# Kernel optimization log

Hardware: AMD Instinct MI355X
Metric: run time of the kernel (lower is better)

## Reference

```python
import jax, jax.numpy as jnp
import numpy as np

B, N, IN_F = 16, 1024, 256
HEADS, OUT_F = 4, 64
NEG_SLOPE = 0.2
CLAMP_MIN = -1e9
MASK_VAL = -9e15


def setup_inputs() -> dict:
    key = jax.random.key(0)
    k1, k2, k3, k4 = jax.random.split(key, 4)
    x = jax.random.normal(k1, (B, N, IN_F), dtype=jnp.float32)
    adj = jax.random.randint(k2, (B, N, N), 0, 2, dtype=jnp.int32)
    # Linear weight, stored as (in, heads*out) so y = x @ W (xavier-uniform scale)
    lim_w = float(np.sqrt(6.0 / (IN_F + HEADS * OUT_F)))
    W = jax.random.uniform(k3, (IN_F, HEADS * OUT_F), dtype=jnp.float32,
                           minval=-lim_w, maxval=lim_w)
    lim_a = float(np.sqrt(6.0 / (2 * OUT_F + HEADS)))
    a = jax.random.uniform(k4, (2 * OUT_F, HEADS), dtype=jnp.float32,
                           minval=-lim_a, maxval=lim_a)
    return {"x": x, "adj": adj, "W": W, "a": a}


def reference(x, adj, W, a):
    Bs, Ns, _ = x.shape
    # Projection: (B,N,H,D)
    h = (x @ W).reshape(Bs, Ns, HEADS, OUT_F)
    # cat([h_i, h_j]) . a == h_i . a_src + h_j . a_dst  (exact same math, no O(N^2*2D) tensor)
    a_src, a_dst = a[:OUT_F], a[OUT_F:]          # each (D, H)
    s_src = jnp.einsum('bnhd,dh->bnh', h, a_src)  # score contribution of node i
    s_dst = jnp.einsum('bnhd,dh->bnh', h, a_dst)  # score contribution of node j
    e = jax.nn.leaky_relu(s_src[:, :, None, :] + s_dst[:, None, :, :],
                          negative_slope=NEG_SLOPE)  # (B,N,N,H)
    # match original: subtract unmasked row max, clamp, then mask, then softmax over j
    e = e - jnp.max(e, axis=2, keepdims=True)
    e = jnp.maximum(e, CLAMP_MIN)
    att = jnp.where(adj[..., None] > 0, e, MASK_VAL)
    att = jax.nn.softmax(att, axis=2)
    h_prime = jnp.einsum('bijh,bjhd->bihd', att, h)  # (B,N,H,D)
    return h_prime.reshape(Bs, Ns, HEADS * OUT_F)
```

## Files before the change

### kernel.cpp

```cpp
#include <hip/hip_runtime.h>
#include <hip/hip_bf16.h>

#define B_   16
#define N_   1024
#define INF_ 256
#define NH_  4
#define HD_  256
#define L2E  1.4426950408889634f

typedef __attribute__((ext_vector_type(8))) short short8;
typedef __attribute__((ext_vector_type(4))) float f32x4;

__device__ __forceinline__ float bf2f(unsigned short u) {
    union { unsigned int i; float f; } v; v.i = ((unsigned int)u) << 16; return v.f;
}
__device__ __forceinline__ unsigned short f2bf(float f) {
    union { float f; unsigned int i; } v; v.f = f;
    unsigned int x = v.i;
    return (unsigned short)((x + 0x7fffu + ((x >> 16) & 1u)) >> 16);
}

__global__ __launch_bounds__(256) void k_prep(const int* __restrict__ adj,
                                              const float* __restrict__ W,
                                              unsigned int* __restrict__ pb,
                                              unsigned short* __restrict__ wswz)
{
    int bx = blockIdx.x, t = threadIdx.x;
    if (bx < 2048) {
        int wave = t >> 6, lane = t & 63;
        int row = bx * 8 + wave * 2 + (lane >> 5);
        int w   = lane & 31;
        const int4* ar = (const int4*)(adj + ((long)row << 10) + w * 32);
        unsigned int u = 0;
        #pragma unroll
        for (int k = 0; k < 8; k++) {
            int4 a = ar[k];
            u |= ((unsigned)a.x) << (4 * k);
            u |= ((unsigned)a.y) << (4 * k + 1);
            u |= ((unsigned)a.z) << (4 * k + 2);
            u |= ((unsigned)a.w) << (4 * k + 3);
        }
        pb[((long)row << 5) + w] = u;
    } else {
        int slot = (bx - 2048) * 256 + t;
        int kstep = slot >> 10;
        int nt    = (slot >> 6) & 15;
        int lane  = slot & 63;
        int k0 = kstep * 32 + (lane >> 4) * 8;
        int n  = nt * 16 + (lane & 15);
        ushort4 o0, o1;
        o0.x = f2bf(W[(k0 + 0) * HD_ + n]);
        o0.y = f2bf(W[(k0 + 1) * HD_ + n]);
        o0.z = f2bf(W[(k0 + 2) * HD_ + n]);
        o0.w = f2bf(W[(k0 + 3) * HD_ + n]);
        o1.x = f2bf(W[(k0 + 4) * HD_ + n]);
        o1.y = f2bf(W[(k0 + 5) * HD_ + n]);
        o1.z = f2bf(W[(k0 + 6) * HD_ + n]);
        o1.w = f2bf(W[(k0 + 7) * HD_ + n]);
        *(ushort4*)&wswz[(long)slot * 8]     = o0;
        *(ushort4*)&wswz[(long)slot * 8 + 4] = o1;
    }
}

__global__ __launch_bounds__(256) void k_gemm_h(
    const float* __restrict__ x, const float* __restrict__ a,
    const unsigned short* __restrict__ wswz,
    unsigned short* __restrict__ hswz,
    float* __restrict__ ssrc, float* __restrict__ sdst)
{
    __shared__ unsigned short xls[16][264];
    int t = threadIdx.x;
    int blk = blockIdx.x;
    int row0 = blk * 16;
    int b  = blk >> 6;
    int n0 = row0 & 1023;

    {
        int sr = t >> 4, sc = (t & 15) * 16;
        const float* xp = x + (long)(row0 + sr) * INF_ + sc;
        float4 v0 = ((const float4*)xp)[0];
        float4 v1 = ((const float4*)xp)[1];
        float4 v2 = ((const float4*)xp)[2];
        float4 v3 = ((const float4*)xp)[3];
        ushort4 u0 = {f2bf(v0.x), f2bf(v0.y), f2bf(v0.z), f2bf(v0.w)};
        ushort4 u1 = {f2bf(v1.x), f2bf(v1.y), f2bf(v1.z), f2bf(v1.w)};
        ushort4 u2 = {f2bf(v2.x), f2bf(v2.y), f2bf(v2.z), f2bf(v2.w)};
        ushort4 u3 = {f2bf(v3.x), f2bf(v3.y), f2bf(v3.z), f2bf(v3.w)};
        *(ushort4*)&xls[sr][sc]      = u0;
        *(ushort4*)&xls[sr][sc + 4]  = u1;
        *(ushort4*)&xls[sr][sc + 8]  = u2;
        *(ushort4*)&xls[sr][sc + 12] = u3;
    }
    __syncthreads();

    int wave = t >> 6, lane = t & 63, quad = lane >> 4, l15 = lane & 15;
    f32x4 acc[4];
    #pragma unroll
    for (int i = 0; i < 4; i++) acc[i] = (f32x4){0.f, 0.f, 0.f, 0.f};

    #pragma unroll
    for (int ks = 0; ks < 8; ks++) {
        short8 af = *(const short8*)&xls[l15][ks * 32 + quad * 8];
        #pragma unroll
        for (int nt = 0; nt < 4; nt++) {
            short8 bf = *(const short8*)(wswz +
                ((long)((ks * 16 + wave * 4 + nt) * 64 + lane)) * 8);
            acc[nt] = __builtin_amdgcn_mfma_f32_16x16x32_bf16(af, bf, acc[nt], 0, 0, 0);
        }
    }

    int q0 = (quad & 1) * 4;
    int qd = ((row0 & 31) + quad * 4) >> 3;
    long bj32 = row0 >> 5;
    #pragma unroll
    for (int nt = 0; nt < 4; nt++) {
        int dg = wave * 4 + nt;
        long idx8 = (bj32 * 16 + dg) * 64 + qd * 16 + l15;
        ushort4 o = {f2bf(acc[nt][0]), f2bf(acc[nt][1]),
                     f2bf(acc[nt][2]), f2bf(acc[nt][3])};
        *(ushort4*)&hswz[idx8 * 8 + q0] = o;
    }

    float as_[4], ad_[4];
    #pragma unroll
    for (int nt = 0; nt < 4; nt++) {
        int d = nt * 16 + l15;
        as_[nt] = a[d * NH_ + wave];
        ad_[nt] = a[(64 + d) * NH_ + wave];
    }
    #pragma unroll
    for (int r = 0; r < 4; r++) {
        float ps = acc[0][r] * as_[0] + acc[1][r] * as_[1]
                 + acc[2][r] * as_[2] + acc[3][r] * as_[3];
        float pd = acc[0][r] * ad_[0] + acc[1][r] * ad_[1]
                 + acc[2][r] * ad_[2] + acc[3][r] * ad_[3];
        #pragma unroll
        for (int m = 1; m < 16; m <<= 1) {
            ps += __shfl_xor(ps, m);
            pd += __shfl_xor(pd, m);
        }
        if (l15 == 0) {
            int row = n0 + quad * 4 + r;
            ssrc[((long)b * NH_ + wave) * N_ + row] = ps * L2E;
            sdst[((long)b * NH_ + wave) * N_ + row] = pd * L2E;
        }
    }
}

__global__ __launch_bounds__(512, 4) void k_attn(
    const unsigned int* __restrict__ pb, const unsigned short* __restrict__ hswz,
    const float* __restrict__ ssrc, const float* __restrict__ sdst,
    float* __restrict__ out)
{
    __shared__ float ss_s[4][32];
    __shared__ float accb[4][2][64][20];

    int t = threadIdx.x;
    int b  = blockIdx.x >> 5, ig = blockIdx.x & 31;
    int i0 = ig * 32;
    int wave = t >> 6, lane = t & 63, quad = lane >> 4, l15 = lane & 15;
    int hh = wave & 3, jh = wave >> 2;

    if (t < 128) {
        int h = t >> 5, i = t & 31;
        ss_s[h][i] = ssrc[((long)(b * NH_ + h)) * N_ + i0 + i];
    }
    __syncthreads();

    float ss0 = ss_s[hh][l15];
    float ss1 = ss_s[hh][16 + l15];
    const float* sdp = sdst + ((long)(b * NH_ + hh)) * N_ + jh * 512;
    long grow0 = ((long)b << 10) + i0 + l15;
    const unsigned int* pb0 = pb + (grow0 << 5) + jh * 16;
    const unsigned int* pb1 = pb0 + (16 << 5);

    f32x4 acc0[4], acc1[4], dn0, dn1;
    #pragma unroll
    for (int i = 0; i < 4; i++) {
        acc0[i] = (f32x4){0.f, 0.f, 0.f, 0.f};
        acc1[i] = (f32x4){0.f, 0.f, 0.f, 0.f};
    }
    dn0 = (f32x4){0.f, 0.f, 0.f, 0.f};
    dn1 = (f32x4){0.f, 0.f, 0.f, 0.f};
    short8 ones;
    #pragma unroll
    for (int i = 0; i < 8; i++) ones[i] = (short)0x3F80;

    int shq = quad * 8;

    #pragma unroll 4
    for (int jc = 0; jc < 16; jc++) {
        unsigned int m0 = (pb0[jc] >> shq) & 0xffu;
        unsigned int m1 = (pb1[jc] >> shq) & 0xffu;
        const float* sj = sdp + jc * 32 + quad * 8;
        float4 sA = *(const float4*)sj;
        float4 sB = *(const float4*)(sj + 4);
        float sv[8] = {sA.x, sA.y, sA.z, sA.w, sB.x, sB.y, sB.z, sB.w};

        union { unsigned int u[4]; short8 s; } p0, p1;
        #pragma unroll
        for (int qp = 0; qp < 4; qp++) {
            unsigned int wb[2][2];
            #pragma unroll
            for (int hv = 0; hv < 2; hv++) {
                int q = 2 * qp + hv;
                float e0 = ss0 + sv[q];
                float w0 = __builtin_exp2f(fmaxf(e0, 0.2f * e0));
                w0 = ((m0 >> q) & 1u) ? w0 : 0.f;
                float e1 = ss1 + sv[q];
                float w1 = __builtin_exp2f(fmaxf(e1, 0.2f * e1));
                w1 = ((m1 >> q) & 1u) ? w1 : 0.f;
                wb[0][hv] = __float_as_uint(w0) + 0x8000u;
                wb[1][hv] = __float_as_uint(w1) + 0x8000u;
            }
            p0.u[qp] = (wb[0][1] & 0xffff0000u) | (wb[0][0] >> 16);
            p1.u[qp] = (wb[1][1] & 0xffff0000u) | (wb[1][0] >> 16);
        }

        long s8 = ((long)(b * 32 + jh * 16 + jc)) * 1024;
        #pragma unroll
        for (int idt = 0; idt < 4; idt++) {
            short8 bf = *(const short8*)(hswz + (s8 + (hh * 4 + idt) * 64 + lane) * 8);
            acc0[idt] = __builtin_amdgcn_mfma_f32_16x16x32_bf16(p0.s, bf, acc0[idt], 0, 0, 0);
            acc1[idt] = __builtin_amdgcn_mfma_f32_16x16x32_bf16(p1.s, bf, acc1[idt], 0, 0, 0);
        }
        dn0 = __builtin_amdgcn_mfma_f32_16x16x32_bf16(p0.s, ones, dn0, 0, 0, 0);
        dn1 = __builtin_amdgcn_mfma_f32_16x16x32_bf16(p1.s, ones, dn1, 0, 0, 0);
    }

    if (jh == 1) {
        #pragma unroll
        for (int idt = 0; idt < 4; idt++) {
            *(f32x4*)&accb[hh][0][lane][idt * 4] = acc0[idt];
            *(f32x4*)&accb[hh][1][lane][idt * 4] = acc1[idt];
        }
        *(f32x4*)&accb[hh][0][lane][16] = dn0;
        *(f32x4*)&accb[hh][1][lane][16] = dn1;
    }
    __syncthreads();

    if (jh == 0) {
        f32x4 od0 = *(const f32x4*)&accb[hh][0][lane][16];
        f32x4 od1 = *(const f32x4*)&accb[hh][1][lane][16];
        float inv0[4], inv1[4];
        #pragma unroll
        for (int r = 0; r < 4; r++) {
            inv0[r] = 1.0f / (dn0[r] + od0[r]);
            inv1[r] = 1.0f / (dn1[r] + od1[r]);
        }
        #pragma unroll
        for (int idt = 0; idt < 4; idt++) {
            f32x4 o0 = *(const f32x4*)&accb[hh][0][lane][idt * 4];
            f32x4 o1 = *(const f32x4*)&accb[hh][1][lane][idt * 4];
            int col = hh * 64 + idt * 16 + l15;
            #pragma unroll
            for (int r = 0; r < 4; r++) {
                long row_g = (long)b * N_ + i0 + quad * 4 + r;
                out[row_g * HD_ + col] = (acc0[idt][r] + o0[r]) * inv0[r];
                out[(row_g + 16) * HD_ + col] = (acc1[idt][r] + o1[r]) * inv1[r];
            }
        }
    }
}

extern "C" void kernel_launch(void* const* d_in, const int* in_sizes, int n_in,
                              void* d_out, int out_size, void* d_ws, size_t ws_size,
                              hipStream_t stream) {
    const float* x   = (const float*)d_in[0];
    const int*   adj = (const int*)d_in[1];
    const float* W   = (const float*)d_in[2];
    const float* a   = (const float*)d_in[3];
    float* out = (float*)d_out;

    unsigned int* pb      = (unsigned int*)d_ws;
    unsigned short* hswz  = (unsigned short*)(pb + 524288);
    unsigned short* wswz  = hswz + (long)B_ * N_ * HD_;
    float* ssrc = (float*)(wswz + INF_ * HD_);
    float* sdst = ssrc + (long)B_ * NH_ * N_;

    k_prep<<<2080, 256, 0, stream>>>(adj, W, pb, wswz);
    k_gemm_h<<<1024, 256, 0, stream>>>(x, a, wswz, hswz, ssrc, sdst);
    k_attn<<<512, 512, 0, stream>>>(pb, hswz, ssrc, sdst, out);
}
```

Measured before the change: 156.1 us.

## Factor exp of leaky-relu scores into per-node exponentials and mask via lookup

The per-edge attention weight exp2(leaky(s_i+s_j)) is rewritten as max(exp2(s_i)*exp2(s_j), exp2(0.2 s_i)*exp2(0.2 s_j)). This holds because exp2 is monotone. The per-node exponentials are computed once in the projection kernel, so the attention inner loop no longer needs transcendental ops. The fp32-to-bf16 packing now uses the hardware v_cvt_pk_bf16_f32 instruction instead of manual rounding. Adjacency masking is applied by ANDing the packed bf16 pairs with a small shared-memory lookup table rather than per-element selects. The trade-off is that computing the two factors separately can overflow or underflow sooner than the fused exponent when scores are large.

```diff
diff --git a/kernel.cpp b/kernel.cpp
--- a/kernel.cpp
+++ b/kernel.cpp
@@ -18,6 +18,11 @@
     union { float f; unsigned int i; } v; v.f = f;
     unsigned int x = v.i;
     return (unsigned short)((x + 0x7fffu + ((x >> 16) & 1u)) >> 16);
+}
+__device__ __forceinline__ unsigned int cvt_pk_bf16(float lo, float hi) {
+    unsigned int r;
+    asm("v_cvt_pk_bf16_f32 %0, %1, %2" : "=v"(r) : "v"(lo), "v"(hi));
+    return r;
 }
 
 __global__ __launch_bounds__(256) void k_prep(const int* __restrict__ adj,
@@ -66,7 +71,7 @@
     const float* __restrict__ x, const float* __restrict__ a,
     const unsigned short* __restrict__ wswz,
     unsigned short* __restrict__ hswz,
-    float* __restrict__ ssrc, float* __restrict__ sdst)
+    float2* __restrict__ esrc, float2* __restrict__ edst)
 {
     __shared__ unsigned short xls[16][264];
     int t = threadIdx.x;
@@ -141,18 +146,22 @@
         }
         if (l15 == 0) {
             int row = n0 + quad * 4 + r;
-            ssrc[((long)b * NH_ + wave) * N_ + row] = ps * L2E;
-            sdst[((long)b * NH_ + wave) * N_ + row] = pd * L2E;
+            float s1 = ps * L2E, s2 = pd * L2E;
+            esrc[((long)b * NH_ + wave) * N_ + row] =
+                make_float2(__builtin_exp2f(s1), __builtin_exp2f(0.2f * s1));
+            edst[((long)b * NH_ + wave) * N_ + row] =
+                make_float2(__builtin_exp2f(s2), __builtin_exp2f(0.2f * s2));
         }
     }
 }
 
 __global__ __launch_bounds__(512, 4) void k_attn(
     const unsigned int* __restrict__ pb, const unsigned short* __restrict__ hswz,
-    const float* __restrict__ ssrc, const float* __restrict__ sdst,
+    const float2* __restrict__ esrc, const float2* __restrict__ edst,
     float* __restrict__ out)
 {
-    __shared__ float ss_s[4][32];
+    __shared__ float2 es_s[4][32];
+    __shared__ uint2 mtab[16];
     __shared__ float accb[4][2][64][20];
 
     int t = threadIdx.x;
@@ -163,13 +172,19 @@
 
     if (t < 128) {
         int h = t >> 5, i = t & 31;
-        ss_s[h][i] = ssrc[((long)(b * NH_ + h)) * N_ + i0 + i];
+        es_s[h][i] = esrc[((long)(b * NH_ + h)) * N_ + i0 + i];
+    }
+    if (t >= 128 && t < 144) {
+        int k = t - 128;
+        unsigned int w0 = ((k & 1) ? 0xffffu : 0u) | ((k & 2) ? 0xffff0000u : 0u);
+        unsigned int w1 = ((k & 4) ? 0xffffu : 0u) | ((k & 8) ? 0xffff0000u : 0u);
+        mtab[k] = make_uint2(w0, w1);
     }
     __syncthreads();
 
-    float ss0 = ss_s[hh][l15];
-    float ss1 = ss_s[hh][16 + l15];
-    const float* sdp = sdst + ((long)(b * NH_ + hh)) * N_ + jh * 512;
+    float2 es0 = es_s[hh][l15];
+    float2 es1 = es_s[hh][16 + l15];
+    const float2* edp = edst + ((long)(b * NH_ + hh)) * N_ + jh * 512;
     long grow0 = ((long)b << 10) + i0 + l15;
     const unsigned int* pb0 = pb + (grow0 << 5) + jh * 16;
     const unsigned int* pb1 = pb0 + (16 << 5);
@@ -192,30 +207,23 @@
     for (int jc = 0; jc < 16; jc++) {
         unsigned int m0 = (pb0[jc] >> shq) & 0xffu;
         unsigned int m1 = (pb1[jc] >> shq) & 0xffu;
-        const float* sj = sdp + jc * 32 + quad * 8;
-        float4 sA = *(const float4*)sj;
-        float4 sB = *(const float4*)(sj + 4);
-        float sv[8] = {sA.x, sA.y, sA.z, sA.w, sB.x, sB.y, sB.z, sB.w};
+        const float4* ej = (const float4*)(edp + jc * 32 + quad * 8);
 
         union { unsigned int u[4]; short8 s; } p0, p1;
         #pragma unroll
         for (int qp = 0; qp < 4; qp++) {
-            unsigned int wb[2][2];
-            #pragma unroll
-            for (int hv = 0; hv < 2; hv++) {
-                int q = 2 * qp + hv;
-                float e0 = ss0 + sv[q];
-                float w0 = __builtin_exp2f(fmaxf(e0, 0.2f * e0));
-                w0 = ((m0 >> q) & 1u) ? w0 : 0.f;
-                float e1 = ss1 + sv[q];
-                float w1 = __builtin_exp2f(fmaxf(e1, 0.2f * e1));
-                w1 = ((m1 >> q) & 1u) ? w1 : 0.f;
-                wb[0][hv] = __float_as_uint(w0) + 0x8000u;
-                wb[1][hv] = __float_as_uint(w1) + 0x8000u;
-            }
-            p0.u[qp] = (wb[0][1] & 0xffff0000u) | (wb[0][0] >> 16);
-            p1.u[qp] = (wb[1][1] & 0xffff0000u) | (wb[1][0] >> 16);
-        }
+            float4 d = ej[qp];
+            float lo0 = fmaxf(es0.x * d.x, es0.y * d.y);
+            float hi0 = fmaxf(es0.x * d.z, es0.y * d.w);
+            float lo1 = fmaxf(es1.x * d.x, es1.y * d.y);
+            float hi1 = fmaxf(es1.x * d.z, es1.y * d.w);
+            p0.u[qp] = cvt_pk_bf16(lo0, hi0);
+            p1.u[qp] = cvt_pk_bf16(lo1, hi1);
+        }
+        uint2 ma0 = mtab[m0 & 15u], mb0 = mtab[m0 >> 4];
+        uint2 ma1 = mtab[m1 & 15u], mb1 = mtab[m1 >> 4];
+        p0.u[0] &= ma0.x; p0.u[1] &= ma0.y; p0.u[2] &= mb0.x; p0.u[3] &= mb0.y;
+        p1.u[0] &= ma1.x; p1.u[1] &= ma1.y; p1.u[2] &= mb1.x; p1.u[3] &= mb1.y;
 
         long s8 = ((long)(b * 32 + jh * 16 + jc)) * 1024;
         #pragma unroll
@@ -275,10 +283,10 @@
     unsigned int* pb      = (unsigned int*)d_ws;
     unsigned short* hswz  = (unsigned short*)(pb + 524288);
     unsigned short* wswz  = hswz + (long)B_ * N_ * HD_;
-    float* ssrc = (float*)(wswz + INF_ * HD_);
-    float* sdst = ssrc + (long)B_ * NH_ * N_;
+    float2* esrc = (float2*)(wswz + INF_ * HD_);
+    float2* edst = esrc + (long)B_ * NH_ * N_;
 
     k_prep<<<2080, 256, 0, stream>>>(adj, W, pb, wswz);
-    k_gemm_h<<<1024, 256, 0, stream>>>(x, a, wswz, hswz, ssrc, sdst);
-    k_attn<<<512, 512, 0, stream>>>(pb, hswz, ssrc, sdst, out);
-}
+    k_gemm_h<<<1024, 256, 0, stream>>>(x, a, wswz, hswz, esrc, edst);
+    k_attn<<<512, 512, 0, stream>>>(pb, hswz, esrc, edst, out);
+}
```

Result: no change. 155.0 us (-0.7%).
